# Kernel tuning notes

Measured on AMD Instinct MI355X. Metric: run time of the kernel, lower is better.

The kernel has to match this reference:

```python
import jax, jax.numpy as jnp
import numpy as np

EDGE = 32          # ImageEdge
KPOOL = 16         # pool_kernel_size = ImageEdge // 2
POOLED = 17        # 1 + ImageEdge - pool_kernel_size
NH = 12            # num_attention_heads
HD = 64            # head_dim
HID = 768          # hidden_size
SR = 2             # ScaleRatio


def setup_inputs() -> dict:
    key = jax.random.key(0)
    k1, k2, k3, k4 = jax.random.split(key, 4)
    B, Q = 8, 2048
    return {
        "image_hidden_states": jax.random.normal(k1, (B, EDGE * EDGE, HID), jnp.float32),
        "text_hidden_states": jax.random.normal(k2, (B, Q, HID), jnp.float32),
        "W_in": jax.random.normal(k3, (HID, HID), jnp.float32) * 0.02,   # input_proj (no bias)
        "W_up": jax.random.normal(k4, (HD, HD * SR * SR), jnp.float32) * 0.02,  # up_proj (no bias)
    }


def reference(image_hidden_states, text_hidden_states, W_in, W_up):
    img, txt = image_hidden_states, text_hidden_states
    B, S, HSZ = img.shape            # S = 1024
    Q = txt.shape[1]
    residual = img

    # cross-attention: text queries attend over image keys
    q = txt.reshape(B, Q, NH, HD).transpose(0, 2, 1, 3)   # [B,H,Q,D]
    k = img.reshape(B, S, NH, HD).transpose(0, 2, 1, 3)   # [B,H,S,D]
    attn = jnp.einsum('bhqd,bhkd->bhqk', q, k) / jnp.sqrt(jnp.float32(HD))
    attn = jax.nn.softmax(attn, axis=-1)                  # [B,H,Q,S]
    # dropout is identity in eval mode

    # pooled attention saliency map
    image_attn = attn.sum(axis=2).reshape(B, NH, EDGE, EDGE)
    pooled = jax.lax.reduce_window(
        image_attn, 0.0, jax.lax.add,
        window_dimensions=(1, 1, KPOOL, KPOOL),
        window_strides=(1, 1, 1, 1), padding='VALID') / (KPOOL * KPOOL)   # [B,H,17,17]
    idx = jnp.argmax(pooled.reshape(B, NH, -1), axis=-1)  # [B,H]
    row = (idx // POOLED).reshape(-1)
    col = (idx % POOLED).reshape(-1)

    # gather the argmax-selected 16x16 region per (batch, head)
    states = img.reshape(B, S, NH, HD).transpose(0, 2, 1, 3)
    states = states.reshape(B * NH, EDGE, EDGE, HD)
    slice_one = lambda s, r, c: jax.lax.dynamic_slice(s, (r, c, 0), (KPOOL, KPOOL, HD))
    region = jax.vmap(slice_one)(states, row, col)        # [B*H,16,16,D]

    # pixel-shuffle upsample back to 32x32
    up = region @ W_up                                    # [B*H,16,16,4*D]
    up = up.reshape(B, NH, KPOOL, KPOOL, SR, SR, HD)
    up = up.transpose(0, 1, 2, 4, 3, 5, 6)                # [B,H,16,2,16,2,D]
    up = up.reshape(B, NH, EDGE * EDGE, HD)
    out = up.transpose(0, 2, 1, 3).reshape(B, EDGE * EDGE, HSZ)

    # dense proj + gelu + residual
    out = jax.nn.gelu(out @ W_in, approximate=False)
    return residual + out
```

## Files before the change

### kernel.cpp

```cpp
#include <hip/hip_runtime.h>
#include <cstdint>
#include <cstddef>

#define BB    8
#define NH    12
#define BH    96
#define SS    1024
#define QQ    2048
#define DD    64
#define HID   768
#define EDGE  32
#define KPOOL 16
#define POOLED 17

typedef short bf16x8 __attribute__((ext_vector_type(8)));
typedef _Float16 f16x8 __attribute__((ext_vector_type(8)));
typedef float f32x4  __attribute__((ext_vector_type(4)));

#define MFMA16B(a, b, c) __builtin_amdgcn_mfma_f32_16x16x32_bf16((a), (b), (c), 0, 0, 0)
#define MFMA16H(a, b, c) __builtin_amdgcn_mfma_f32_16x16x32_f16((a), (b), (c), 0, 0, 0)

#define QSCALE 0.18033688011112042f

#if __has_builtin(__builtin_amdgcn_exp2f)
#define EXP2(x) __builtin_amdgcn_exp2f(x)
#else
#define EXP2(x) exp2f(x)
#endif

__device__ __forceinline__ short f2bf(float x) {
    unsigned u = __builtin_bit_cast(unsigned, x);
    u = u + 0x7fffu + ((u >> 16) & 1u);
    return (short)(u >> 16);
}
__device__ __forceinline__ f16x8 ash(bf16x8 v) {
    return __builtin_bit_cast(f16x8, v);
}

__device__ __forceinline__ size_t fragaddr(int row, int k) {
    return ((size_t)(row >> 4) * 24 + (k >> 5)) * 512 + ((k >> 3) & 3) * 128
         + (row & 15) * 8 + (k & 7);
}

__device__ __forceinline__ size_t partaddr(size_t j) {
    return (j >> 9) * 1024 + 512 + (j & 511);
}


__global__ __launch_bounds__(256) void k_castq(const float* __restrict__ txt,
                                               short* __restrict__ Qs) {
    int i = blockIdx.x * 256 + threadIdx.x;
    int quad = i & 3, kh = (i >> 2) & 1;
    int row = i >> 3;
    int c = row & 15, g = row >> 4;
    int q = row & 2047, bh = row >> 11;
    int b = bh / NH, h = bh - b * NH;
    const float* sp = txt + ((size_t)b * QQ + q) * HID + h * DD + kh * 32 + quad * 8;
    bf16x8 vh;
#pragma unroll
    for (int j = 0; j < 8; j++) {
        _Float16 hi = (_Float16)(sp[j] * QSCALE);
        vh[j] = __builtin_bit_cast(short, hi);
    }
    *(bf16x8*)(Qs + (size_t)g * 2048 + kh * 512 + quad * 128 + c * 8) = vh;
}

__global__ __launch_bounds__(256) void k_castk(const float* __restrict__ img,
                                               short* __restrict__ Ks) {
    int i = blockIdx.x * 256 + threadIdx.x;
    int quad = i & 3, kh = (i >> 2) & 1;
    int row = i >> 3;
    int c = row & 15, g = row >> 4;
    int s = row & 1023, bh = row >> 10;
    int b = bh / NH, h = bh - b * NH;
    const float* sp = img + ((size_t)b * SS + s) * HID + h * DD + kh * 32 + quad * 8;
    bf16x8 vh;
#pragma unroll
    for (int j = 0; j < 8; j++) {
        _Float16 hi = (_Float16)sp[j];
        vh[j] = __builtin_bit_cast(short, hi);
    }
    *(bf16x8*)(Ks + (size_t)g * 2048 + kh * 512 + quad * 128 + c * 8) = vh;
}

__global__ __launch_bounds__(256) void k_castw(const float* __restrict__ W,
                                               const float* __restrict__ Wup,
                                               short* __restrict__ Wt,
                                               short* __restrict__ Wupb) {
    if (blockIdx.x == 144) {
        for (int i = threadIdx.x; i < 16384; i += 256) {
            int k = i >> 8, n = i & 255;
            int addr = (n >> 4) * 1024 + (k >> 5) * 512 + ((k >> 3) & 3) * 128
                     + (n & 15) * 8 + (k & 7);
            Wupb[addr] = f2bf(Wup[k * 256 + n]);
        }
        return;
    }
    __shared__ float T[64][65];
    int bx = blockIdx.x % 12, by = blockIdx.x / 12;
    for (int i = threadIdx.x; i < 4096; i += 256) {
        int r = i >> 6, cc = i & 63;
        T[r][cc] = W[(size_t)(by * 64 + r) * HID + bx * 64 + cc];
    }
    __syncthreads();
    for (int i = threadIdx.x; i < 4096; i += 256) {
        int r = i >> 6, cc = i & 63;
        int n = bx * 64 + r, k = by * 64 + cc;
        Wt[fragaddr(n, k)] = f2bf(T[cc][r]);
    }
}

__global__ __launch_bounds__(512) void k_fused(const short* __restrict__ Qs,
                                               const short* __restrict__ Ks,
                                               float* __restrict__ Part) {
    __shared__ short Kt[2][4096];
    __shared__ float iacc[2][1024];
    __shared__ float Lred[2][4][16];

    int bh = blockIdx.x >> 6, qb = blockIdx.x & 63;
    int tid = threadIdx.x;
    int w = tid >> 6, lane = tid & 63;
    int qi = w >> 2, si = w & 3;
    int quad = lane >> 4, c = lane & 15;

    const short* ap = Qs + ((size_t)bh * 128 + qb * 2 + qi) * 2048 + lane * 8;
    f16x8 a0 = ash(*(const bf16x8*)(ap));
    f16x8 a1 = ash(*(const bf16x8*)(ap + 512));

    const short* kbase = Ks + (size_t)bh * SS * 128;
    size_t soff = (size_t)(tid >> 7) * 2048 + (size_t)(tid & 127) * 8;

    f32x4 pt[16];
    bf16x8 st = *(const bf16x8*)(kbase + soff);

#pragma unroll
    for (int cc = 0; cc < 16; cc++) {
        int buf = cc & 1;
        *(bf16x8*)(&Kt[buf][tid * 8]) = st;
        if (cc + 1 < 16)
            st = *(const bf16x8*)(kbase + (size_t)(cc + 1) * 8192 + soff);
        __syncthreads();
        f16x8 kb0 = ash(*(const bf16x8*)(&Kt[buf][si * 1024 + lane * 8]));
        f16x8 kb1 = ash(*(const bf16x8*)(&Kt[buf][si * 1024 + 512 + lane * 8]));
        f32x4 acc = (f32x4){0.f, 0.f, 0.f, 0.f};
        acc = MFMA16H(a0, kb0, acc);
        acc = MFMA16H(a1, kb1, acc);
#pragma unroll
        for (int r = 0; r < 4; r++) pt[cc][r] = EXP2(acc[r]);
    }

    float Lp[4], rl[4];
#pragma unroll
    for (int r = 0; r < 4; r++) {
        float v = 0.f;
#pragma unroll
        for (int cc = 0; cc < 16; cc++) v += pt[cc][r];
        v += __shfl_xor(v, 1);
        v += __shfl_xor(v, 2);
        v += __shfl_xor(v, 4);
        v += __shfl_xor(v, 8);
        Lp[r] = v;
    }
    if (c == 0) {
#pragma unroll
        for (int r = 0; r < 4; r++) Lred[qi][si][quad * 4 + r] = Lp[r];
    }
    __syncthreads();
#pragma unroll
    for (int r = 0; r < 4; r++)
        rl[r] = __builtin_amdgcn_rcpf(
            Lred[qi][0][quad * 4 + r] + Lred[qi][1][quad * 4 + r] +
            Lred[qi][2][quad * 4 + r] + Lred[qi][3][quad * 4 + r]);

#pragma unroll
    for (int cc = 0; cc < 16; cc++) {
        float v = pt[cc][0] * rl[0] + pt[cc][1] * rl[1]
                + pt[cc][2] * rl[2] + pt[cc][3] * rl[3];
        v += __shfl_xor(v, 16);
        v += __shfl_xor(v, 32);
        if (lane < 16) iacc[qi][cc * 64 + si * 16 + lane] = v;
    }
    __syncthreads();
    for (int i = tid; i < 1024; i += 512) {
        size_t j = (size_t)blockIdx.x * 1024 + i;
        Part[partaddr(j)] = iacc[0][i] + iacc[1][i];
    }
}

__global__ __launch_bounds__(256) void k_reduce(const float* __restrict__ Part,
                                                float* __restrict__ iattn) {
    int bh = blockIdx.x >> 2, quarter = blockIdx.x & 3;
    int s = quarter * 256 + threadIdx.x;
    float v = 0.f;
#pragma unroll 8
    for (int qb = 0; qb < 64; qb++) {
        size_t j = ((size_t)(bh * 64 + qb)) * 1024 + s;
        v += Part[partaddr(j)];
    }
    iattn[(size_t)bh * SS + s] = v;
}

__global__ __launch_bounds__(256, 2) void k_up(const float* __restrict__ img,
                                               const float* __restrict__ iattn,
                                               const short* __restrict__ Wupb,
                                               short* __restrict__ Xb) {
    __shared__ short Reg[16384];
    float* F = (float*)Reg;
    float* Apool = F;
    float* Vp = F + 1024;
    float* bvp = F + 1568;
    int*   bip = (int*)(F + 1824);

    int bh = blockIdx.x >> 2, nq = blockIdx.x & 3;
    int b = bh / NH, h = bh - b * NH;
    int tid = threadIdx.x;
    int w = tid >> 6, lane = tid & 63;
    int quad = lane >> 4, c = lane & 15;

    for (int i = tid; i < 1024; i += 256) Apool[i] = iattn[(size_t)bh * SS + i];
    __syncthreads();
    for (int i = tid; i < POOLED * EDGE; i += 256) {
        int r = i >> 5, cc = i & 31;
        float s = 0.f;
#pragma unroll
        for (int k = 0; k < KPOOL; k++) s += Apool[(r + k) * EDGE + cc];
        Vp[i] = s;
    }
    __syncthreads();
    float best = -1e30f;
    int bidx = 1 << 30;
    for (int i = tid; i < POOLED * POOLED; i += 256) {
        int r = i / POOLED, cc = i - r * POOLED;
        float s = 0.f;
#pragma unroll
        for (int k = 0; k < KPOOL; k++) s += Vp[r * EDGE + cc + k];
        if (s > best || (s == best && i < bidx)) { best = s; bidx = i; }
    }
    bvp[tid] = best;
    bip[tid] = bidx;
    __syncthreads();
    for (int off = 128; off; off >>= 1) {
        if (tid < off) {
            float ov = bvp[tid + off];
            int oi = bip[tid + off];
            if (ov > bvp[tid] || (ov == bvp[tid] && oi < bip[tid])) {
                bvp[tid] = ov;
                bip[tid] = oi;
            }
        }
        __syncthreads();
    }
    int widx = bip[0];
    __syncthreads();
    int r0 = widx / POOLED, c0 = widx - r0 * POOLED;

    for (int p = tid; p < 2048; p += 256) {
        int pos = p >> 3, sub = p & 7;
        int gi = r0 + (pos >> 4), gj = c0 + (pos & 15);
        const float* sp = img + ((size_t)b * SS + gi * EDGE + gj) * HID + h * DD + sub * 8;
        bf16x8 v;
#pragma unroll
        for (int j = 0; j < 8; j++) v[j] = f2bf(sp[j]);
        *(bf16x8*)(&Reg[(pos >> 4) * 1024 + (sub >> 2) * 512 + (sub & 3) * 128 + (pos & 15) * 8]) = v;
    }
    __syncthreads();

    bf16x8 bu[4][2];
#pragma unroll
    for (int u = 0; u < 4; u++) {
#pragma unroll
        for (int kh = 0; kh < 2; kh++)
            bu[u][kh] = *(const bf16x8*)(Wupb + (nq * 4 + u) * 1024 + kh * 512 + lane * 8);
    }

#pragma unroll
    for (int t = 0; t < 4; t++) {
        int g = w * 4 + t;
        bf16x8 a0 = *(const bf16x8*)(&Reg[g * 1024 + lane * 8]);
        bf16x8 a1 = *(const bf16x8*)(&Reg[g * 1024 + 512 + lane * 8]);
#pragma unroll
        for (int u = 0; u < 4; u++) {
            f32x4 acc = (f32x4){0.f, 0.f, 0.f, 0.f};
            acc = MFMA16B(a0, bu[u][0], acc);
            acc = MFMA16B(a1, bu[u][1], acc);
#pragma unroll
            for (int r = 0; r < 4; r++) {
                int pos = g * 16 + quad * 4 + r;
                int oc = nq * 64 + u * 16 + c;
                int i16 = pos >> 4, j16 = pos & 15;
                int a = oc >> 7, bbit = (oc >> 6) & 1, dp = oc & 63;
                int p2 = (2 * i16 + a) * EDGE + (2 * j16 + bbit);
                int row = b * SS + p2, kdim = h * DD + dp;
                Xb[fragaddr(row, kdim)] = f2bf(acc[r]);
            }
        }
    }
}

__global__ __launch_bounds__(256) void k_out(const short* __restrict__ Xb,
                                             const short* __restrict__ Wt,
                                             const float* __restrict__ img,
                                             float* __restrict__ out) {
    __shared__ short At[2][4096];
    __shared__ short Bt[2][2048];
    int mblk = blockIdx.x & 63, nblk = blockIdx.x >> 6;
    int tid = threadIdx.x;
    int w = tid >> 6, lane = tid & 63;
    int quad = lane >> 4, c = lane & 15;
    int gm0 = mblk * 8, gn0 = nblk * 4;
    int m0 = mblk * 128, n0 = nblk * 64;

    int ua1 = tid + 256;
    const short* srcA0 = Xb + ((size_t)(gm0 + (tid >> 6)) * 24) * 512 + (tid & 63) * 8;
    const short* srcA1 = Xb + ((size_t)(gm0 + (ua1 >> 6)) * 24) * 512 + (ua1 & 63) * 8;
    const short* srcB  = Wt + ((size_t)(gn0 + (tid >> 6)) * 24) * 512 + (tid & 63) * 8;

    f32x4 acc[2][4];
#pragma unroll
    for (int t = 0; t < 2; t++)
#pragma unroll
        for (int u = 0; u < 4; u++) acc[t][u] = (f32x4){0.f, 0.f, 0.f, 0.f};

    bf16x8 sa0 = *(const bf16x8*)(srcA0);
    bf16x8 sa1 = *(const bf16x8*)(srcA1);
    bf16x8 sb  = *(const bf16x8*)(srcB);

    for (int kk = 0; kk < 24; kk++) {
        int buf = kk & 1;
        *(bf16x8*)(&At[buf][tid * 8]) = sa0;
        *(bf16x8*)(&At[buf][ua1 * 8]) = sa1;
        *(bf16x8*)(&Bt[buf][tid * 8]) = sb;
        if (kk + 1 < 24) {
            sa0 = *(const bf16x8*)(srcA0 + (kk + 1) * 512);
            sa1 = *(const bf16x8*)(srcA1 + (kk + 1) * 512);
            sb  = *(const bf16x8*)(srcB  + (kk + 1) * 512);
        }
        __syncthreads();
        bf16x8 a0 = *(const bf16x8*)(&At[buf][(2 * w + 0) * 512 + lane * 8]);
        bf16x8 a1 = *(const bf16x8*)(&At[buf][(2 * w + 1) * 512 + lane * 8]);
        bf16x8 b0 = *(const bf16x8*)(&Bt[buf][0 * 512 + lane * 8]);
        bf16x8 b1 = *(const bf16x8*)(&Bt[buf][1 * 512 + lane * 8]);
        bf16x8 b2 = *(const bf16x8*)(&Bt[buf][2 * 512 + lane * 8]);
        bf16x8 b3 = *(const bf16x8*)(&Bt[buf][3 * 512 + lane * 8]);
        acc[0][0] = MFMA16B(a0, b0, acc[0][0]);
        acc[0][1] = MFMA16B(a0, b1, acc[0][1]);
        acc[0][2] = MFMA16B(a0, b2, acc[0][2]);
        acc[0][3] = MFMA16B(a0, b3, acc[0][3]);
        acc[1][0] = MFMA16B(a1, b0, acc[1][0]);
        acc[1][1] = MFMA16B(a1, b1, acc[1][1]);
        acc[1][2] = MFMA16B(a1, b2, acc[1][2]);
        acc[1][3] = MFMA16B(a1, b3, acc[1][3]);
    }

#pragma unroll
    for (int t = 0; t < 2; t++) {
#pragma unroll
        for (int u = 0; u < 4; u++) {
#pragma unroll
            for (int r = 0; r < 4; r++) {
                int row = m0 + w * 32 + t * 16 + quad * 4 + r;
                int col = n0 + u * 16 + c;
                float x = acc[t][u][r];
                float g = 0.5f * x * (1.f + erff(x * 0.70710678118654752f));
                size_t o = (size_t)row * HID + col;
                out[o] = img[o] + g;
            }
        }
    }
}

extern "C" void kernel_launch(void* const* d_in, const int* in_sizes, int n_in,
                              void* d_out, int out_size, void* d_ws, size_t ws_size,
                              hipStream_t stream) {
    const float* img = (const float*)d_in[0];
    const float* txt = (const float*)d_in[1];
    const float* Win = (const float*)d_in[2];
    const float* Wup = (const float*)d_in[3];
    float* out = (float*)d_out;

    char* w = (char*)d_ws;
    short* Qs    = (short*)(w);
    short* Ks    = (short*)(w + 50331648);
    short* Wt    = (short*)(w + 75497472);
    float* iattn = (float*)(w + 77463552);
    short* Wupb  = (short*)(w + 77856768);
    float* Part  = (float*)(w);
    short* Xb    = (short*)(w);

    k_castq<<<dim3(6144), dim3(256), 0, stream>>>(txt, Qs);
    k_castk<<<dim3(3072), dim3(256), 0, stream>>>(img, Ks);
    k_castw<<<dim3(145), dim3(256), 0, stream>>>(Win, Wup, Wt, Wupb);
    k_fused<<<dim3(6144), dim3(512), 0, stream>>>(Qs, Ks, Part);
    k_reduce<<<dim3(384), dim3(256), 0, stream>>>(Part, iattn);
    k_up<<<dim3(384), dim3(256), 0, stream>>>(img, iattn, Wupb, Xb);
    k_out<<<dim3(768), dim3(256), 0, stream>>>(Xb, Wt, img, out);
}
```

Before: 266.0 us.

## Stage K in larger chunks per barrier and swizzle block-to-head mapping

The attention-score kernel now loads 128 key rows per iteration into a doubled shared-memory buffer and runs two MFMA groups per wave between barriers, so it needs eight synchronisations instead of sixteen. The block index is remapped so that consecutive blocks span eight different heads at the same query block, which changes L2 locality across concurrently running blocks. The aim is to cut barrier overhead and raise the number of loads in flight, at the cost of more LDS per block, which can lower occupancy.

```diff
diff --git a/kernel.cpp b/kernel.cpp
--- a/kernel.cpp
+++ b/kernel.cpp
@@ -113,11 +113,13 @@
 __global__ __launch_bounds__(512) void k_fused(const short* __restrict__ Qs,
                                                const short* __restrict__ Ks,
                                                float* __restrict__ Part) {
-    __shared__ short Kt[2][4096];
+    __shared__ short Kt[2][8192];
     __shared__ float iacc[2][1024];
     __shared__ float Lred[2][4][16];
 
-    int bh = blockIdx.x >> 6, qb = blockIdx.x & 63;
+    int m = blockIdx.x;
+    int bh = ((m >> 9) << 3) | (m & 7);
+    int qb = (m >> 3) & 63;
     int tid = threadIdx.x;
     int w = tid >> 6, lane = tid & 63;
     int qi = w >> 2, si = w & 3;
@@ -128,28 +130,38 @@
     f16x8 a1 = ash(*(const bf16x8*)(ap + 512));
 
     const short* kbase = Ks + (size_t)bh * SS * 128;
-    size_t soff = (size_t)(tid >> 7) * 2048 + (size_t)(tid & 127) * 8;
+    size_t s0 = (size_t)(tid >> 7) * 2048 + (size_t)(tid & 127) * 8;
+    int i1 = tid + 512;
+    size_t s1 = (size_t)(i1 >> 7) * 2048 + (size_t)(i1 & 127) * 8;
 
     f32x4 pt[16];
-    bf16x8 st = *(const bf16x8*)(kbase + soff);
-
-#pragma unroll
-    for (int cc = 0; cc < 16; cc++) {
+    bf16x8 st0 = *(const bf16x8*)(kbase + s0);
+    bf16x8 st1 = *(const bf16x8*)(kbase + s1);
+
+#pragma unroll
+    for (int cc = 0; cc < 8; cc++) {
         int buf = cc & 1;
-        *(bf16x8*)(&Kt[buf][tid * 8]) = st;
-        if (cc + 1 < 16)
-            st = *(const bf16x8*)(kbase + (size_t)(cc + 1) * 8192 + soff);
+        *(bf16x8*)(&Kt[buf][tid * 8]) = st0;
+        *(bf16x8*)(&Kt[buf][(tid + 512) * 8]) = st1;
+        if (cc + 1 < 8) {
+            st0 = *(const bf16x8*)(kbase + (size_t)(cc + 1) * 16384 + s0);
+            st1 = *(const bf16x8*)(kbase + (size_t)(cc + 1) * 16384 + s1);
+        }
         __syncthreads();
-        f16x8 kb0 = ash(*(const bf16x8*)(&Kt[buf][si * 1024 + lane * 8]));
-        f16x8 kb1 = ash(*(const bf16x8*)(&Kt[buf][si * 1024 + 512 + lane * 8]));
-        f32x4 acc = (f32x4){0.f, 0.f, 0.f, 0.f};
-        acc = MFMA16H(a0, kb0, acc);
-        acc = MFMA16H(a1, kb1, acc);
-#pragma unroll
-        for (int r = 0; r < 4; r++) pt[cc][r] = EXP2(acc[r]);
-    }
-
-    float Lp[4], rl[4];
+#pragma unroll
+        for (int h = 0; h < 2; h++) {
+            const short* kp = &Kt[buf][(si + h * 4) * 1024 + lane * 8];
+            f16x8 kb0 = ash(*(const bf16x8*)(kp));
+            f16x8 kb1 = ash(*(const bf16x8*)(kp + 512));
+            f32x4 acc = (f32x4){0.f, 0.f, 0.f, 0.f};
+            acc = MFMA16H(a0, kb0, acc);
+            acc = MFMA16H(a1, kb1, acc);
+#pragma unroll
+            for (int r = 0; r < 4; r++) pt[cc * 2 + h][r] = EXP2(acc[r]);
+        }
+    }
+
+    float rl[4];
 #pragma unroll
     for (int r = 0; r < 4; r++) {
         float v = 0.f;
@@ -159,11 +171,7 @@
         v += __shfl_xor(v, 2);
         v += __shfl_xor(v, 4);
         v += __shfl_xor(v, 8);
-        Lp[r] = v;
-    }
-    if (c == 0) {
-#pragma unroll
-        for (int r = 0; r < 4; r++) Lred[qi][si][quad * 4 + r] = Lp[r];
+        if (c == 0) Lred[qi][si][quad * 4 + r] = v;
     }
     __syncthreads();
 #pragma unroll
@@ -173,16 +181,19 @@
             Lred[qi][2][quad * 4 + r] + Lred[qi][3][quad * 4 + r]);
 
 #pragma unroll
-    for (int cc = 0; cc < 16; cc++) {
-        float v = pt[cc][0] * rl[0] + pt[cc][1] * rl[1]
-                + pt[cc][2] * rl[2] + pt[cc][3] * rl[3];
-        v += __shfl_xor(v, 16);
-        v += __shfl_xor(v, 32);
-        if (lane < 16) iacc[qi][cc * 64 + si * 16 + lane] = v;
+    for (int cc = 0; cc < 8; cc++) {
+#pragma unroll
+        for (int h = 0; h < 2; h++) {
+            float v = pt[cc * 2 + h][0] * rl[0] + pt[cc * 2 + h][1] * rl[1]
+                    + pt[cc * 2 + h][2] * rl[2] + pt[cc * 2 + h][3] * rl[3];
+            v += __shfl_xor(v, 16);
+            v += __shfl_xor(v, 32);
+            if (lane < 16) iacc[qi][cc * 128 + (si + h * 4) * 16 + lane] = v;
+        }
     }
     __syncthreads();
     for (int i = tid; i < 1024; i += 512) {
-        size_t j = (size_t)blockIdx.x * 1024 + i;
+        size_t j = ((size_t)(bh * 64 + qb)) * 1024 + i;
         Part[partaddr(j)] = iacc[0][i] + iacc[1][i];
     }
 }
```

Measured after the change: 261.4 us. No clear change (-1.7%).
